# Kernel optimization log

Hardware: AMD Instinct MI355X
Metric: run time of the kernel (lower is better)

The kernel has to match this reference:

```python
import jax, jax.numpy as jnp
import numpy as np

N_NODES = 50000
N_EDGES = 1600000
IN_F = 256
OUT_F = 128
N_REL = 500
NEG_SLOPE = 0.2
EPS = 1e-10


def setup_inputs() -> dict:
    key = jax.random.key(0)
    ks = jax.random.split(key, 7)
    h = jax.random.normal(ks[0], (N_NODES, IN_F), dtype=jnp.float32)
    rows = jax.random.randint(ks[1], (N_EDGES,), 0, N_NODES)
    cols = jax.random.randint(ks[2], (N_EDGES,), 0, N_NODES)
    edge_types = jax.random.randint(ks[3], (N_EDGES,), 0, N_REL)
    # learned params (xavier-ish small scale)
    W = jax.random.normal(ks[4], (IN_F, OUT_F), dtype=jnp.float32) * 0.05
    rel_emb = jax.random.normal(ks[5], (N_REL, OUT_F), dtype=jnp.float32) * 0.05
    a = jax.random.normal(ks[6], (2 * OUT_F + OUT_F,), dtype=jnp.float32) * 0.05
    return {"h": h, "rows": rows, "cols": cols, "edge_types": edge_types,
            "W": W, "rel_emb": rel_emb, "a": a}


def reference(h, rows, cols, edge_types, W, rel_emb, a):
    N = h.shape[0]
    d = W.shape[1]
    Wh = h @ W                                   # [N, out]
    # a^T [Wh_i || Wh_j || r] decomposed to avoid materializing the concat
    a_i, a_j, a_r = a[:d], a[d:2 * d], a[2 * d:]
    s_node_i = Wh @ a_i                          # [N]
    s_node_j = Wh @ a_j                          # [N]
    s_rel = rel_emb @ a_r                        # [R]
    e = s_node_i[rows] + s_node_j[cols] + s_rel[edge_types]   # [E]
    e = jax.nn.leaky_relu(e, negative_slope=NEG_SLOPE)
    e = e - jnp.max(e)                           # global max-shift as in original
    exp_e = jnp.exp(e)
    sum_exp = jax.ops.segment_sum(exp_e, rows, num_segments=N)  # [N]
    alpha = exp_e / (sum_exp[rows] + EPS)        # [E]  (dropout is identity in eval)
    # sparse matmul: h'_i = sum_{j in N(i)} alpha_ij * Wh_j
    h_prime = jax.ops.segment_sum(alpha[:, None] * Wh[cols], rows, num_segments=N)
    return jax.nn.elu(h_prime)
```

## Files before the change

kernel.cpp:

```cpp
#include <hip/hip_runtime.h>

#define N_NODES 50000
#define N_EDGES 1600000
#define IN_F    256
#define OUT_F   128
#define N_REL   500
#define NEG_SLOPE 0.2f
#define EPS_F   1e-10f
#define GEMM_ROWS 64

#define NB       782
#define CAP      2304
#define BIN_CHUNK 4096
#define NBIN_BLK 391
#define PREP_BLK 189

typedef __attribute__((ext_vector_type(8))) __bf16 bf16x8;
typedef __attribute__((ext_vector_type(4))) float f32x4;
typedef __attribute__((ext_vector_type(2))) float f32x2;

static __device__ __forceinline__ float bf2f(unsigned short u) {
    unsigned v = ((unsigned)u) << 16;
    float f;
    __builtin_memcpy(&f, &v, 4);
    return f;
}
static __device__ __forceinline__ unsigned short f2bf(float f) {
    unsigned u;
    __builtin_memcpy(&u, &f, 4);
    unsigned rounding = 0x7fffu + ((u >> 16) & 1u);
    u += rounding;
    return (unsigned short)(u >> 16);
}

__global__ __launch_bounds__(256) void prep_k(
    const float* __restrict__ W,
    const float* __restrict__ a,
    const float* __restrict__ rel_emb,
    unsigned short* __restrict__ WbfT,
    unsigned short* __restrict__ wai_bf, unsigned short* __restrict__ waj_bf,
    float* __restrict__ s_rel,
    int* __restrict__ cnt)
{
    int gi = blockIdx.x * 256 + threadIdx.x;
    if (gi < NB) cnt[gi << 4] = 0;

    int wid  = threadIdx.x >> 6;
    int lane = threadIdx.x & 63;
    if (blockIdx.x < 64) {
        int k    = blockIdx.x * 4 + wid;
        int n0   = lane * 2;
        float2 wv2 = *(const float2*)(W + (size_t)k * OUT_F + n0);
        WbfT[(size_t)n0 * IN_F + k]       = f2bf(wv2.x);
        WbfT[(size_t)(n0 + 1) * IN_F + k] = f2bf(wv2.y);
        float si = wv2.x * a[n0] + wv2.y * a[n0 + 1];
        float sj = wv2.x * a[OUT_F + n0] + wv2.y * a[OUT_F + n0 + 1];
        #pragma unroll
        for (int off = 32; off; off >>= 1) {
            si += __shfl_xor(si, off, 64);
            sj += __shfl_xor(sj, off, 64);
        }
        if (lane == 0) { wai_bf[k] = f2bf(si); waj_bf[k] = f2bf(sj); }
    } else {
        int rid = (blockIdx.x - 64) * 4 + wid;
        if (rid >= N_REL) return;
        float2 re = *(const float2*)(rel_emb + (size_t)rid * OUT_F + 2 * lane);
        float2 ar = *(const float2*)(a + 2 * OUT_F + 2 * lane);
        float sr = re.x * ar.x + re.y * ar.y;
        #pragma unroll
        for (int off = 32; off; off >>= 1) sr += __shfl_xor(sr, off, 64);
        if (lane == 0) s_rel[rid] = sr;
    }
}

__global__ __launch_bounds__(256) void gemm_wh(
    const float* __restrict__ h,
    const unsigned short* __restrict__ WbfT,
    const unsigned short* __restrict__ wai_bf, const unsigned short* __restrict__ waj_bf,
    unsigned short* __restrict__ Whb,
    float* __restrict__ s_i, float* __restrict__ s_j)
{
    __shared__ unsigned short Ash[GEMM_ROWS * IN_F];
    const int t    = threadIdx.x;
    const int wv   = t >> 6;
    const int lane = t & 63;
    const int quad = lane >> 4;
    const int l15  = lane & 15;
    const int r0   = blockIdx.x * GEMM_ROWS;

    bf16x8 Bfrag[2][8];
    #pragma unroll
    for (int ct2 = 0; ct2 < 2; ++ct2) {
        int n = 32 * wv + 16 * ct2 + l15;
        #pragma unroll
        for (int ks = 0; ks < 8; ++ks)
            Bfrag[ct2][ks] = *(const bf16x8*)(WbfT + (size_t)n * IN_F + 32 * ks + 8 * quad);
    }
    bf16x8 Sfrag[8];
    if (wv == 0) {
        const unsigned short* ssrc = (l15 == 0) ? wai_bf : waj_bf;
        #pragma unroll
        for (int ks = 0; ks < 8; ++ks) {
            if (l15 < 2) Sfrag[ks] = *(const bf16x8*)(ssrc + 32 * ks + 8 * quad);
            else         Sfrag[ks] = (bf16x8)(__bf16)0.0f;
        }
    }

    #pragma unroll
    for (int i = 0; i < 16; ++i) {
        int q   = t + 256 * i;
        int row = q >> 6;
        int k   = (q & 63) * 4;
        int gr  = r0 + row;
        float4 v = make_float4(0.f, 0.f, 0.f, 0.f);
        if (gr < N_NODES) v = *(const float4*)(h + (size_t)gr * IN_F + k);
        int ks = k >> 5, qd = (k >> 3) & 3, j = k & 7;
        int rg = row >> 4, m15 = row & 15;
        int off = ((((rg << 3) + ks) << 6) + ((qd << 4) | m15)) * 8 + j;
        ushort4 p;
        p.x = f2bf(v.x); p.y = f2bf(v.y); p.z = f2bf(v.z); p.w = f2bf(v.w);
        *(ushort4*)(Ash + off) = p;
    }
    __syncthreads();

    #pragma unroll 1
    for (int rg = 0; rg < 4; ++rg) {
        const unsigned short* base = Ash + (((rg << 3) << 6) + lane) * 8;
        bf16x8 Afrag[8];
        #pragma unroll
        for (int ks = 0; ks < 8; ++ks)
            Afrag[ks] = *(const bf16x8*)(base + (ks << 6) * 8);
        f32x4 acc0 = {0.f, 0.f, 0.f, 0.f};
        f32x4 acc1 = {0.f, 0.f, 0.f, 0.f};
        #pragma unroll
        for (int ks = 0; ks < 8; ++ks) {
            acc0 = __builtin_amdgcn_mfma_f32_16x16x32_bf16(Afrag[ks], Bfrag[0][ks], acc0, 0, 0, 0);
            acc1 = __builtin_amdgcn_mfma_f32_16x16x32_bf16(Afrag[ks], Bfrag[1][ks], acc1, 0, 0, 0);
        }
        #pragma unroll
        for (int reg = 0; reg < 4; ++reg) {
            int gr = r0 + 16 * rg + quad * 4 + reg;
            if (gr < N_NODES) {
                Whb[(size_t)gr * OUT_F + 32 * wv + l15]      = f2bf(acc0[reg]);
                Whb[(size_t)gr * OUT_F + 32 * wv + 16 + l15] = f2bf(acc1[reg]);
            }
        }
        if (wv == 0) {
            f32x4 acc2 = {0.f, 0.f, 0.f, 0.f};
            #pragma unroll
            for (int ks = 0; ks < 8; ++ks)
                acc2 = __builtin_amdgcn_mfma_f32_16x16x32_bf16(Afrag[ks], Sfrag[ks], acc2, 0, 0, 0);
            #pragma unroll
            for (int reg = 0; reg < 4; ++reg) {
                int gr = r0 + 16 * rg + quad * 4 + reg;
                if (gr < N_NODES) {
                    if (l15 == 0) s_i[gr] = acc2[reg];
                    else if (l15 == 1) s_j[gr] = acc2[reg];
                }
            }
        }
    }
}

__global__ __launch_bounds__(256) void bin_k(
    const int* __restrict__ rows, const int* __restrict__ cols, const int* __restrict__ types,
    const float* __restrict__ s_i, const float* __restrict__ s_j, const float* __restrict__ s_rel,
    int* __restrict__ cnt, uint2* __restrict__ epk)
{
    __shared__ int hist[NB];
    __shared__ int lbase[NB];
    __shared__ float srl[N_REL];
    int t = threadIdx.x;
    for (int i = t; i < NB; i += 256) hist[i] = 0;
    for (int i = t; i < N_REL; i += 256) srl[i] = s_rel[i];
    __syncthreads();

    int base = blockIdx.x * BIN_CHUNK;
    float cw[16];
    unsigned cm[16];
    #pragma unroll
    for (int i = 0; i < 16; ++i) {
        int e = base + t + 256 * i;
        if (e < N_EDGES) {
            int r = rows[e], c = cols[e], ty = types[e];
            float v = s_i[r] + s_j[c] + srl[ty];
            v = (v > 0.f) ? v : NEG_SLOPE * v;
            cw[i] = __expf(v);
            int b = r >> 6;
            cm[i] = (unsigned)c | ((unsigned)(r & 63) << 16) | ((unsigned)b << 22);
            atomicAdd(&hist[b], 1);
        } else {
            cw[i] = 0.f;
            cm[i] = 0xffffffffu;
        }
    }
    __syncthreads();
    for (int i = t; i < NB; i += 256)
        if (hist[i] > 0) lbase[i] = atomicAdd(&cnt[i << 4], hist[i]);
    __syncthreads();
    #pragma unroll
    for (int i = 0; i < 16; ++i) {
        if (cm[i] != 0xffffffffu) {
            int b = cm[i] >> 22;
            int loc = lbase[b] + atomicSub(&hist[b], 1) - 1;
            if (loc < CAP)
                epk[(size_t)b * CAP + loc] = make_uint2(__float_as_uint(cw[i]), cm[i] & 0x3fffffu);
        }
    }
}

__global__ __launch_bounds__(256, 8) void bucket_agg(
    const int* __restrict__ cnt, const uint2* __restrict__ epk,
    const unsigned short* __restrict__ Whb,
    float* __restrict__ out)
{
    __shared__ uint2 sorted[CAP];
    __shared__ int hist[64];
    __shared__ int offs[65];
    __shared__ int cur[64];

    const int t    = threadIdx.x;
    const int wid  = t >> 6;
    const int lane = t & 63;
    const int b    = blockIdx.x;
    const int n    = min(cnt[b << 4], CAP);
    const uint2* ep = epk + (size_t)b * CAP;

    if (t < 64) hist[t] = 0;
    __syncthreads();

    uint2 rec[9];
    #pragma unroll
    for (int i = 0; i < 9; ++i) {
        int idx = t + 256 * i;
        rec[i] = (idx < n) ? ep[idx] : make_uint2(0u, 0xffffffffu);
    }
    #pragma unroll
    for (int i = 0; i < 9; ++i)
        if (rec[i].y != 0xffffffffu) atomicAdd(&hist[(rec[i].y >> 16) & 63], 1);
    __syncthreads();
    if (wid == 0) {
        int v = hist[lane];
        #pragma unroll
        for (int off = 1; off < 64; off <<= 1) {
            int u = __shfl_up(v, off, 64);
            if (lane >= off) v += u;
        }
        offs[lane + 1] = v;
        if (lane == 0) offs[0] = 0;
        cur[lane] = v - hist[lane];
    }
    __syncthreads();
    #pragma unroll
    for (int i = 0; i < 9; ++i) {
        if (rec[i].y != 0xffffffffu) {
            int pos = atomicAdd(&cur[(rec[i].y >> 16) & 63], 1);
            sorted[pos] = make_uint2(rec[i].x, (rec[i].y & 0xffffu) << 8);
        }
    }
    __syncthreads();

    const unsigned hh = lane >> 5;
    const unsigned lb = (unsigned)(lane & 31) << 3;
    const char* wbase = (const char*)Whb;

    #pragma unroll 1
    for (int rl = 0; rl < 16; ++rl) {
        const int row = wid * 16 + rl;
        int i = offs[row];
        const int e1 = offs[row + 1];
        f32x2 a01 = {0.f, 0.f};
        f32x2 a23 = {0.f, 0.f};
        float s = 0.f;

        for (; i + 16 <= e1; i += 16) {
            uint2 rc[8];
            #pragma unroll
            for (int j = 0; j < 8; ++j) rc[j] = sorted[i + 2 * j + hh];
            uint2 pk[8];
            #pragma unroll
            for (int j = 0; j < 8; ++j)
                pk[j] = *(const uint2*)(wbase + (rc[j].y + lb));
            __builtin_amdgcn_sched_barrier(0);
            #pragma unroll
            for (int j = 0; j < 8; ++j) {
                float w = __uint_as_float(rc[j].x);
                unsigned p0 = pk[j].x, p1 = pk[j].y;
                a01.x = __builtin_fmaf(__uint_as_float(p0 << 16),          w, a01.x);
                a01.y = __builtin_fmaf(__uint_as_float(p0 & 0xffff0000u),  w, a01.y);
                a23.x = __builtin_fmaf(__uint_as_float(p1 << 16),          w, a23.x);
                a23.y = __builtin_fmaf(__uint_as_float(p1 & 0xffff0000u),  w, a23.y);
                s += w;
            }
        }
        for (; i + 4 <= e1; i += 4) {
            uint2 rc0 = sorted[i + hh];
            uint2 rc1 = sorted[i + 2 + hh];
            uint2 pk0 = *(const uint2*)(wbase + (rc0.y + lb));
            uint2 pk1 = *(const uint2*)(wbase + (rc1.y + lb));
            float w0 = __uint_as_float(rc0.x);
            float w1 = __uint_as_float(rc1.x);
            a01.x = __builtin_fmaf(__uint_as_float(pk0.x << 16),         w0, a01.x);
            a01.y = __builtin_fmaf(__uint_as_float(pk0.x & 0xffff0000u), w0, a01.y);
            a23.x = __builtin_fmaf(__uint_as_float(pk0.y << 16),         w0, a23.x);
            a23.y = __builtin_fmaf(__uint_as_float(pk0.y & 0xffff0000u), w0, a23.y);
            a01.x = __builtin_fmaf(__uint_as_float(pk1.x << 16),         w1, a01.x);
            a01.y = __builtin_fmaf(__uint_as_float(pk1.x & 0xffff0000u), w1, a01.y);
            a23.x = __builtin_fmaf(__uint_as_float(pk1.y << 16),         w1, a23.x);
            a23.y = __builtin_fmaf(__uint_as_float(pk1.y & 0xffff0000u), w1, a23.y);
            s += w0 + w1;
        }
        for (; i < e1; i += 2) {
            int idx = i + (int)hh;
            uint2 r0 = (idx < e1) ? sorted[idx] : make_uint2(0u, 0u);
            uint2 pk0 = *(const uint2*)(wbase + (r0.y + lb));
            float w = __uint_as_float(r0.x);
            a01.x = __builtin_fmaf(__uint_as_float(pk0.x << 16),         w, a01.x);
            a01.y = __builtin_fmaf(__uint_as_float(pk0.x & 0xffff0000u), w, a01.y);
            a23.x = __builtin_fmaf(__uint_as_float(pk0.y << 16),         w, a23.x);
            a23.y = __builtin_fmaf(__uint_as_float(pk0.y & 0xffff0000u), w, a23.y);
            s += w;
        }

        s     += __shfl_xor(s, 32, 64);
        a01.x += __shfl_xor(a01.x, 32, 64);
        a01.y += __shfl_xor(a01.y, 32, 64);
        a23.x += __shfl_xor(a23.x, 32, 64);
        a23.y += __shfl_xor(a23.y, 32, 64);

        if (hh == 0) {
            const int grow = b * 64 + row;
            if (grow < N_NODES) {
                float inv = 1.f / (s + EPS_F);
                float v0 = a01.x * inv, v1 = a01.y * inv;
                float v2 = a23.x * inv, v3 = a23.y * inv;
                v0 = (v0 > 0.f) ? v0 : (__expf(v0) - 1.f);
                v1 = (v1 > 0.f) ? v1 : (__expf(v1) - 1.f);
                v2 = (v2 > 0.f) ? v2 : (__expf(v2) - 1.f);
                v3 = (v3 > 0.f) ? v3 : (__expf(v3) - 1.f);
                *(float4*)(out + (size_t)grow * OUT_F + ((lane & 31) << 2)) =
                    make_float4(v0, v1, v2, v3);
            }
        }
    }
}

extern "C" void kernel_launch(void* const* d_in, const int* in_sizes, int n_in,
                              void* d_out, int out_size, void* d_ws, size_t ws_size,
                              hipStream_t stream)
{
    const float* h     = (const float*)d_in[0];
    const int*   rows  = (const int*)d_in[1];
    const int*   cols  = (const int*)d_in[2];
    const int*   types = (const int*)d_in[3];
    const float* W     = (const float*)d_in[4];
    const float* rel   = (const float*)d_in[5];
    const float* a     = (const float*)d_in[6];

    char* ws = (char*)d_ws;
    size_t off = 0;
    auto alloc = [&](size_t bytes) -> void* {
        void* p = ws + off;
        off = (off + bytes + 255) & ~(size_t)255;
        return p;
    };
    unsigned short* Whb   = (unsigned short*)alloc((size_t)N_NODES * OUT_F * 2);
    unsigned short* WbfT  = (unsigned short*)alloc((size_t)IN_F * OUT_F * 2);
    unsigned short* wai_bf = (unsigned short*)alloc((size_t)IN_F * 2);
    unsigned short* waj_bf = (unsigned short*)alloc((size_t)IN_F * 2);
    float* s_i    = (float*)alloc((size_t)N_NODES * 4);
    float* s_j    = (float*)alloc((size_t)N_NODES * 4);
    float* s_rel  = (float*)alloc((size_t)N_REL * 4);
    int*   cnt    = (int*)alloc((size_t)NB * 16 * 4);
    uint2* epk    = (uint2*)alloc((size_t)NB * CAP * 8);
    (void)ws_size; (void)in_sizes; (void)n_in; (void)out_size;

    prep_k<<<PREP_BLK, 256, 0, stream>>>(W, a, rel, WbfT, wai_bf, waj_bf, s_rel, cnt);
    gemm_wh<<<(N_NODES + GEMM_ROWS - 1) / GEMM_ROWS, 256, 0, stream>>>(
        h, WbfT, wai_bf, waj_bf, Whb, s_i, s_j);
    bin_k<<<NBIN_BLK, 256, 0, stream>>>(rows, cols, types, s_i, s_j, s_rel, cnt, epk);
    bucket_agg<<<NB, 256, 0, stream>>>(cnt, epk, Whb, (float*)d_out);
}
```

Baseline: 225.7 us.

## Split bucket aggregation into four feature slices with four-edge lane groups

The aggregation loop now walks the feature dimension in four 32-column slices. Each slice uses 16 lanes per edge and processes four edges in parallel per wavefront, replacing the earlier layout of 32 lanes per edge with two edges in parallel. The aim is to keep the working set of gathered Wh rows per pass smaller and more cache-friendly, and to raise memory-level parallelism. The cost is re-reading the sorted edge list four times, issuing narrower 4-byte gathers, and adding extra shuffle reductions. Launch bounds occupancy drops from 8 to 4.

```diff
diff --git a/kernel.cpp b/kernel.cpp
--- a/kernel.cpp
+++ b/kernel.cpp
@@ -17,14 +17,7 @@
 
 typedef __attribute__((ext_vector_type(8))) __bf16 bf16x8;
 typedef __attribute__((ext_vector_type(4))) float f32x4;
-typedef __attribute__((ext_vector_type(2))) float f32x2;
-
-static __device__ __forceinline__ float bf2f(unsigned short u) {
-    unsigned v = ((unsigned)u) << 16;
-    float f;
-    __builtin_memcpy(&f, &v, 4);
-    return f;
-}
+
 static __device__ __forceinline__ unsigned short f2bf(float f) {
     unsigned u;
     __builtin_memcpy(&u, &f, 4);
@@ -209,7 +202,7 @@
     }
 }
 
-__global__ __launch_bounds__(256, 8) void bucket_agg(
+__global__ __launch_bounds__(256, 4) void bucket_agg(
     const int* __restrict__ cnt, const uint2* __restrict__ epk,
     const unsigned short* __restrict__ Whb,
     float* __restrict__ out)
@@ -260,86 +253,74 @@
     }
     __syncthreads();
 
-    const unsigned hh = lane >> 5;
-    const unsigned lb = (unsigned)(lane & 31) << 3;
+    const int g  = lane >> 4;
+    const int lg = lane & 15;
     const char* wbase = (const char*)Whb;
 
     #pragma unroll 1
-    for (int rl = 0; rl < 16; ++rl) {
-        const int row = wid * 16 + rl;
-        int i = offs[row];
-        const int e1 = offs[row + 1];
-        f32x2 a01 = {0.f, 0.f};
-        f32x2 a23 = {0.f, 0.f};
-        float s = 0.f;
-
-        for (; i + 16 <= e1; i += 16) {
-            uint2 rc[8];
-            #pragma unroll
-            for (int j = 0; j < 8; ++j) rc[j] = sorted[i + 2 * j + hh];
-            uint2 pk[8];
-            #pragma unroll
-            for (int j = 0; j < 8; ++j)
-                pk[j] = *(const uint2*)(wbase + (rc[j].y + lb));
-            __builtin_amdgcn_sched_barrier(0);
-            #pragma unroll
-            for (int j = 0; j < 8; ++j) {
-                float w = __uint_as_float(rc[j].x);
-                unsigned p0 = pk[j].x, p1 = pk[j].y;
-                a01.x = __builtin_fmaf(__uint_as_float(p0 << 16),          w, a01.x);
-                a01.y = __builtin_fmaf(__uint_as_float(p0 & 0xffff0000u),  w, a01.y);
-                a23.x = __builtin_fmaf(__uint_as_float(p1 << 16),          w, a23.x);
-                a23.y = __builtin_fmaf(__uint_as_float(p1 & 0xffff0000u),  w, a23.y);
+    for (int slice = 0; slice < 4; ++slice) {
+        const unsigned soff = (unsigned)(slice * 64 + lg * 4);
+        #pragma unroll 1
+        for (int rl = 0; rl < 16; ++rl) {
+            const int row = wid * 16 + rl;
+            int i = offs[row];
+            const int e1 = offs[row + 1];
+            float s = 0.f, x0 = 0.f, x1 = 0.f;
+
+            for (; i + 16 <= e1; i += 16) {
+                uint2 rc[4];
+                #pragma unroll
+                for (int q = 0; q < 4; ++q) rc[q] = sorted[i + 4 * q + g];
+                unsigned pk[4];
+                #pragma unroll
+                for (int q = 0; q < 4; ++q)
+                    pk[q] = *(const unsigned*)(wbase + (rc[q].y + soff));
+                __builtin_amdgcn_sched_barrier(0);
+                #pragma unroll
+                for (int q = 0; q < 4; ++q) {
+                    float w = __uint_as_float(rc[q].x);
+                    x0 = __builtin_fmaf(__uint_as_float(pk[q] << 16),         w, x0);
+                    x1 = __builtin_fmaf(__uint_as_float(pk[q] & 0xffff0000u), w, x1);
+                    s += w;
+                }
+            }
+            for (; i + 8 <= e1; i += 8) {
+                uint2 rc0 = sorted[i + g];
+                uint2 rc1 = sorted[i + 4 + g];
+                unsigned pk0 = *(const unsigned*)(wbase + (rc0.y + soff));
+                unsigned pk1 = *(const unsigned*)(wbase + (rc1.y + soff));
+                float w0 = __uint_as_float(rc0.x);
+                float w1 = __uint_as_float(rc1.x);
+                x0 = __builtin_fmaf(__uint_as_float(pk0 << 16),         w0, x0);
+                x1 = __builtin_fmaf(__uint_as_float(pk0 & 0xffff0000u), w0, x1);
+                x0 = __builtin_fmaf(__uint_as_float(pk1 << 16),         w1, x0);
+                x1 = __builtin_fmaf(__uint_as_float(pk1 & 0xffff0000u), w1, x1);
+                s += w0 + w1;
+            }
+            for (; i < e1; i += 4) {
+                int idx = i + g;
+                uint2 r0 = (idx < e1) ? sorted[idx] : make_uint2(0u, 0u);
+                unsigned pk0 = *(const unsigned*)(wbase + (r0.y + soff));
+                float w = __uint_as_float(r0.x);
+                x0 = __builtin_fmaf(__uint_as_float(pk0 << 16),         w, x0);
+                x1 = __builtin_fmaf(__uint_as_float(pk0 & 0xffff0000u), w, x1);
                 s += w;
             }
-        }
-        for (; i + 4 <= e1; i += 4) {
-            uint2 rc0 = sorted[i + hh];
-            uint2 rc1 = sorted[i + 2 + hh];
-            uint2 pk0 = *(const uint2*)(wbase + (rc0.y + lb));
-            uint2 pk1 = *(const uint2*)(wbase + (rc1.y + lb));
-            float w0 = __uint_as_float(rc0.x);
-            float w1 = __uint_as_float(rc1.x);
-            a01.x = __builtin_fmaf(__uint_as_float(pk0.x << 16),         w0, a01.x);
-            a01.y = __builtin_fmaf(__uint_as_float(pk0.x & 0xffff0000u), w0, a01.y);
-            a23.x = __builtin_fmaf(__uint_as_float(pk0.y << 16),         w0, a23.x);
-            a23.y = __builtin_fmaf(__uint_as_float(pk0.y & 0xffff0000u), w0, a23.y);
-            a01.x = __builtin_fmaf(__uint_as_float(pk1.x << 16),         w1, a01.x);
-            a01.y = __builtin_fmaf(__uint_as_float(pk1.x & 0xffff0000u), w1, a01.y);
-            a23.x = __builtin_fmaf(__uint_as_float(pk1.y << 16),         w1, a23.x);
-            a23.y = __builtin_fmaf(__uint_as_float(pk1.y & 0xffff0000u), w1, a23.y);
-            s += w0 + w1;
-        }
-        for (; i < e1; i += 2) {
-            int idx = i + (int)hh;
-            uint2 r0 = (idx < e1) ? sorted[idx] : make_uint2(0u, 0u);
-            uint2 pk0 = *(const uint2*)(wbase + (r0.y + lb));
-            float w = __uint_as_float(r0.x);
-            a01.x = __builtin_fmaf(__uint_as_float(pk0.x << 16),         w, a01.x);
-            a01.y = __builtin_fmaf(__uint_as_float(pk0.x & 0xffff0000u), w, a01.y);
-            a23.x = __builtin_fmaf(__uint_as_float(pk0.y << 16),         w, a23.x);
-            a23.y = __builtin_fmaf(__uint_as_float(pk0.y & 0xffff0000u), w, a23.y);
-            s += w;
-        }
-
-        s     += __shfl_xor(s, 32, 64);
-        a01.x += __shfl_xor(a01.x, 32, 64);
-        a01.y += __shfl_xor(a01.y, 32, 64);
-        a23.x += __shfl_xor(a23.x, 32, 64);
-        a23.y += __shfl_xor(a23.y, 32, 64);
-
-        if (hh == 0) {
-            const int grow = b * 64 + row;
-            if (grow < N_NODES) {
-                float inv = 1.f / (s + EPS_F);
-                float v0 = a01.x * inv, v1 = a01.y * inv;
-                float v2 = a23.x * inv, v3 = a23.y * inv;
-                v0 = (v0 > 0.f) ? v0 : (__expf(v0) - 1.f);
-                v1 = (v1 > 0.f) ? v1 : (__expf(v1) - 1.f);
-                v2 = (v2 > 0.f) ? v2 : (__expf(v2) - 1.f);
-                v3 = (v3 > 0.f) ? v3 : (__expf(v3) - 1.f);
-                *(float4*)(out + (size_t)grow * OUT_F + ((lane & 31) << 2)) =
-                    make_float4(v0, v1, v2, v3);
+
+            s  += __shfl_xor(s, 16, 64);  s  += __shfl_xor(s, 32, 64);
+            x0 += __shfl_xor(x0, 16, 64); x0 += __shfl_xor(x0, 32, 64);
+            x1 += __shfl_xor(x1, 16, 64); x1 += __shfl_xor(x1, 32, 64);
+
+            if (g == 0) {
+                const int grow = b * 64 + row;
+                if (grow < N_NODES) {
+                    float inv = 1.f / (s + EPS_F);
+                    float v0 = x0 * inv, v1 = x1 * inv;
+                    v0 = (v0 > 0.f) ? v0 : (__expf(v0) - 1.f);
+                    v1 = (v1 > 0.f) ? v1 : (__expf(v1) - 1.f);
+                    *(float2*)(out + (size_t)grow * OUT_F + slice * 32 + 2 * lg) =
+                        make_float2(v0, v1);
+                }
             }
         }
     }
```

New measurement: 281.0 us. 1.25x slower.
